# Performance work log

Hardware: AMD Instinct MI355X
Metric: run time of the kernel (lower is better)

## Reference

```python
import jax, jax.numpy as jnp
import numpy as np

N = 100000   # nodes
E = 1600000  # edges
G = 512      # graphs
ATOM = 64
HID = 64
CLS = 10


def layer_norm(x, g, b, eps=1e-5):
    mu = jnp.mean(x, axis=-1, keepdims=True)
    var = jnp.mean((x - mu) ** 2, axis=-1, keepdims=True)
    return (x - mu) * jax.lax.rsqrt(var + eps) * g + b


def gcn_conv(x, src, dst, W, b, fill, num_nodes):
    # PyG GCNConv with add_self_loops: A_hat = A + fill*I, sym-normalized.
    h = x @ W                                            # [N, F_out]
    ones = jnp.ones(src.shape[0], dtype=h.dtype)
    deg = jax.ops.segment_sum(ones, dst, num_segments=num_nodes) + fill
    dinv = jax.lax.rsqrt(deg)                            # deg^{-1/2}
    norm = dinv[src] * dinv[dst]                         # [E]
    msg = h[src] * norm[:, None]                         # gather + scale
    out = jax.ops.segment_sum(msg, dst, num_segments=num_nodes)
    out = out + (fill * dinv * dinv)[:, None] * h        # self-loop term
    return out + b


def setup_inputs() -> dict:
    key = jax.random.key(0)
    ks = jax.random.split(key, 8)
    x = jax.random.normal(ks[0], (N, ATOM), dtype=jnp.float32)
    edge_index = jax.random.randint(ks[1], (2, E), 0, N, dtype=jnp.int64)
    batch = jnp.sort(jax.random.randint(ks[2], (N,), 0, G, dtype=jnp.int64))
    s = lambda k, sh, fan: jax.random.normal(k, sh, jnp.float32) / np.sqrt(fan)
    return {
        "x": x, "edge_index": edge_index, "batch": batch,
        "W1": s(ks[3], (ATOM, HID), ATOM), "b1": jnp.zeros((HID,), jnp.float32),
        "ln_g": jnp.ones((HID,), jnp.float32), "ln_b": jnp.zeros((HID,), jnp.float32),
        "W2": s(ks[4], (HID, HID), HID), "b2": jnp.zeros((HID,), jnp.float32),
        "W3": s(ks[5], (HID, 768), HID), "b3": jnp.zeros((768,), jnp.float32),
        "ln2_g": jnp.ones((768,), jnp.float32), "ln2_b": jnp.zeros((768,), jnp.float32),
        "W4": s(ks[6], (768, CLS), 768), "b4": jnp.zeros((CLS,), jnp.float32),
    }


def reference(x, edge_index, batch, W1, b1, ln_g, ln_b, W2, b2,
              W3, b3, ln2_g, ln2_b, W4, b4):
    src, dst = edge_index[0], edge_index[1]
    leaky = lambda v: jax.nn.leaky_relu(v, 0.2)
    # GCN1 (improved=True -> self-loop weight 2.0) + LN + LeakyReLU
    h = gcn_conv(x, src, dst, W1, b1, 2.0, N)
    h = leaky(layer_norm(h, ln_g, ln_b))
    # GCN2 (self-loop weight 1.0) + LeakyReLU
    h = gcn_conv(h, src, dst, W2, b2, 1.0, N)
    h = leaky(h)
    # global max pool over graphs
    pooled = jax.ops.segment_max(h, batch, num_segments=G)  # [G, HID]
    # seq2 head (Dropout is identity at inference)
    z = pooled @ W3 + b3
    z = leaky(layer_norm(z, ln2_g, ln2_b))
    z = z @ W4 + b4
    return jax.nn.softmax(z, axis=-1)
```

## Files before the change

### kernel.cpp

```cpp
#include <hip/hip_runtime.h>
#include <hip/hip_bf16.h>

#define NODES 100000
#define EDGES 1600000
#define NGRAPH 512
#define NBINS 98
#define CHUNK 4096
#define VSS 72

using bf16 = __hip_bfloat16;
typedef long long ll;
using frag8 = __attribute__((ext_vector_type(8))) short;
using f32x4 = __attribute__((ext_vector_type(4))) float;

__device__ __forceinline__ float lrelu(float v) { return v > 0.0f ? v : 0.2f * v; }

__device__ __forceinline__ unsigned mapf(float f) {
    unsigned u = __float_as_uint(f);
    return (u & 0x80000000u) ? ~u : (u | 0x80000000u);
}
__device__ __forceinline__ float unmapf(unsigned u) {
    return __uint_as_float((u & 0x80000000u) ? (u ^ 0x80000000u) : ~u);
}

__device__ __forceinline__ int idx_at(const void* raw, int i, int f) {
    return f ? (int)((const ll*)raw)[i] : ((const int*)raw)[i];
}

__device__ __forceinline__ unsigned short tobf(float f) {
    bf16 h = __float2bfloat16(f);
    return *reinterpret_cast<unsigned short*>(&h);
}

__global__ void sentinel_kernel(float* out, float v) {
    int i = blockIdx.x * blockDim.x + threadIdx.x;
    if (i < NGRAPH * 10) out[i] = v;
}

__global__ void detect_init(const int* __restrict__ w, int* __restrict__ flag,
                            unsigned* __restrict__ pooled, int* __restrict__ binTotal,
                            int* __restrict__ binCursor) {
    int i = blockIdx.x * blockDim.x + threadIdx.x;
    if (i < NGRAPH * 64) pooled[i] = mapf(-1e4f);
    if (i < NBINS) { binTotal[i] = 0; binCursor[i] = 0; }
    if (blockIdx.x == 0) {
        __shared__ int red[4];
        int t = threadIdx.x;
        int v = 0;
        for (int k = t; k < 4096; k += 256) v |= w[2 * k + 1];
        for (int o = 32; o; o >>= 1) v |= __shfl_xor(v, o);
        if ((t & 63) == 0) red[t >> 6] = v;
        __syncthreads();
        if (t == 0) flag[0] = ((red[0] | red[1] | red[2] | red[3]) == 0) ? 1 : 0;
    }
}

__global__ void binCount(const void* __restrict__ ei, const int* __restrict__ flag,
                         int* __restrict__ binTotal) {
    __shared__ int hist[NBINS];
    int t = threadIdx.x;
    if (t < NBINS) hist[t] = 0;
    __syncthreads();
    int e0 = blockIdx.x * CHUNK;
    int f = flag[0];
#pragma unroll
    for (int k = 0; k < CHUNK / 256; ++k) {
        int i = e0 + k * 256 + t;
        if (i < EDGES) {
            int s = idx_at(ei, i, f), d = idx_at(ei, EDGES + i, f);
            if ((unsigned)s < NODES && (unsigned)d < NODES) atomicAdd(&hist[d >> 10], 1);
        }
    }
    __syncthreads();
    if (t < NBINS && hist[t] > 0) atomicAdd(&binTotal[t], hist[t]);
}

__global__ void scan98(const int* __restrict__ binTotal, int* __restrict__ binStart,
                       int* __restrict__ row_ptr) {
    __shared__ int sc[128];
    int t = threadIdx.x;
    int v = (t < NBINS) ? binTotal[t] : 0;
    sc[t] = v;
    __syncthreads();
    for (int o = 1; o < 128; o <<= 1) {
        int u = (t >= o) ? sc[t - o] : 0;
        __syncthreads();
        sc[t] += u;
        __syncthreads();
    }
    if (t < NBINS) binStart[t] = sc[t] - v;
    if (t == NBINS - 1) {
        binStart[NBINS] = sc[t];
        row_ptr[NODES] = sc[t];
    }
}

__global__ void binPlace(const void* __restrict__ ei, const int* __restrict__ flag,
                         const int* __restrict__ binStart, int* __restrict__ binCursor,
                         unsigned* __restrict__ staging) {
    __shared__ unsigned recs[CHUNK];
    __shared__ unsigned char binsA[CHUNK];
    __shared__ int hist[NBINS], lstart[NBINS + 1], baseg[NBINS], lcur[NBINS];
    int t = threadIdx.x;
    if (t < NBINS) { hist[t] = 0; lcur[t] = 0; }
    __syncthreads();
    int e0 = blockIdx.x * CHUNK;
    int f = flag[0];
#pragma unroll
    for (int k = 0; k < CHUNK / 256; ++k) {
        int i = e0 + k * 256 + t;
        if (i < EDGES) {
            int s = idx_at(ei, i, f), d = idx_at(ei, EDGES + i, f);
            if ((unsigned)s < NODES && (unsigned)d < NODES) atomicAdd(&hist[d >> 10], 1);
        }
    }
    __syncthreads();
    if (t == 0) {
        int acc = 0;
        for (int b = 0; b < NBINS; ++b) {
            lstart[b] = acc;
            acc += hist[b];
        }
        lstart[NBINS] = acc;
    }
    __syncthreads();
    if (t < NBINS && hist[t] > 0) baseg[t] = atomicAdd(&binCursor[t], hist[t]);
    __syncthreads();
#pragma unroll
    for (int k = 0; k < CHUNK / 256; ++k) {
        int i = e0 + k * 256 + t;
        if (i < EDGES) {
            int s = idx_at(ei, i, f), d = idx_at(ei, EDGES + i, f);
            if ((unsigned)s < NODES && (unsigned)d < NODES) {
                int b = d >> 10;
                int p = lstart[b] + atomicAdd(&lcur[b], 1);
                recs[p] = ((unsigned)s << 10) | (unsigned)(d & 1023);
                binsA[p] = (unsigned char)b;
            }
        }
    }
    __syncthreads();
    int nv = lstart[NBINS];
    for (int p = t; p < nv; p += 256) {
        int b = binsA[p];
        staging[binStart[b] + baseg[b] + (p - lstart[b])] = recs[p];
    }
}

__global__ void csr_finalize(const unsigned* __restrict__ staging,
                             const int* __restrict__ binStart, int* __restrict__ row_ptr,
                             float* __restrict__ dinv1, float* __restrict__ dinv2,
                             int* __restrict__ csr_src) {
    __shared__ int lhist[1024];
    __shared__ int sc[256];
    int b = blockIdx.x, t = threadIdx.x;
    int r0 = b << 10;
    int s0 = binStart[b], s1 = binStart[b + 1];
    for (int j = t; j < 1024; j += 256) lhist[j] = 0;
    __syncthreads();
    for (int p = s0 + t; p < s1; p += 256) atomicAdd(&lhist[staging[p] & 1023], 1);
    __syncthreads();
    int base = t * 4;
    int v0 = lhist[base], v1 = lhist[base + 1], v2 = lhist[base + 2], v3 = lhist[base + 3];
    int tsum = v0 + v1 + v2 + v3;
    sc[t] = tsum;
    __syncthreads();
    for (int o = 1; o < 256; o <<= 1) {
        int u = (t >= o) ? sc[t - o] : 0;
        __syncthreads();
        sc[t] += u;
        __syncthreads();
    }
    int excl = sc[t] - tsum;
    int vv0 = v0, vv1 = v1, vv2 = v2, vv3 = v3;
    int ex[4];
    ex[0] = excl;
    ex[1] = excl + vv0;
    ex[2] = ex[1] + vv1;
    ex[3] = ex[2] + vv2;
    int vvs[4] = {vv0, vv1, vv2, vv3};
#pragma unroll
    for (int k = 0; k < 4; ++k) {
        int j = base + k;
        int row = r0 + j;
        if (row < NODES) {
            row_ptr[row] = s0 + ex[k];
            float dg = (float)vvs[k];
            dinv1[row] = 1.0f / sqrtf(dg + 2.0f);
            dinv2[row] = 1.0f / sqrtf(dg + 1.0f);
        }
    }
    __syncthreads();
#pragma unroll
    for (int k = 0; k < 4; ++k) lhist[base + k] = ex[k];
    __syncthreads();
    for (int p = s0 + t; p < s1; p += 256) {
        unsigned rec = staging[p];
        int dl = rec & 1023;
        int slot = atomicAdd(&lhist[dl], 1);
        csr_src[s0 + slot] = (int)(rec >> 10);
    }
}

__global__ void prescale_x(const float* __restrict__ x, const float* __restrict__ dinv1,
                           bf16* __restrict__ xs) {
    int i = blockIdx.x * blockDim.x + threadIdx.x;
    if (i < NODES * 64) xs[i] = __float2bfloat16(x[i] * dinv1[i >> 6]);
}

__device__ __forceinline__ void gather_quad(const uint2* __restrict__ feat4,
                                            const int* __restrict__ csr, int beg, int end,
                                            int lane, float& ox, float& oy, float& oz,
                                            float& ow) {
    int q = lane >> 4, c = lane & 15;
    float ax = 0, ay = 0, az = 0, aw = 0;
    float bx = 0, by = 0, bz = 0, bw = 0;
    for (int cb = beg; cb < end; cb += 64) {
        int cnt = min(64, end - cb);
        int idx = (cb + lane < end) ? csr[cb + lane] : 0;
        for (int j = 0; j < cnt; j += 8) {
            int e0 = j + q, e1 = j + 4 + q;
            int s0 = __shfl(idx, e0);
            uint2 u0 = feat4[(size_t)s0 * 16 + c];
            if (e0 < cnt) {
                ax += __uint_as_float(u0.x << 16);
                ay += __uint_as_float(u0.x & 0xffff0000u);
                az += __uint_as_float(u0.y << 16);
                aw += __uint_as_float(u0.y & 0xffff0000u);
            }
            if (j + 4 < cnt) {
                int s1 = __shfl(idx, e1);
                uint2 u1 = feat4[(size_t)s1 * 16 + c];
                if (e1 < cnt) {
                    bx += __uint_as_float(u1.x << 16);
                    by += __uint_as_float(u1.x & 0xffff0000u);
                    bz += __uint_as_float(u1.y << 16);
                    bw += __uint_as_float(u1.y & 0xffff0000u);
                }
            }
        }
    }
    ax += bx; ay += by; az += bz; aw += bw;
    ax += __shfl_xor(ax, 16); ay += __shfl_xor(ay, 16);
    az += __shfl_xor(az, 16); aw += __shfl_xor(aw, 16);
    ax += __shfl_xor(ax, 32); ay += __shfl_xor(ay, 32);
    az += __shfl_xor(az, 32); aw += __shfl_xor(aw, 32);
    ox = ax; oy = ay; oz = az; ow = aw;
}

__device__ __forceinline__ void gcn_core(const uint2* __restrict__ feat4,
                                         const int* __restrict__ csr,
                                         const int* __restrict__ rp,
                                         const float* __restrict__ dinv, float selfw,
                                         const float* __restrict__ W, short* Vs, short* Wt,
                                         int rowBase, int lane, int wave, f32x4 (&acc)[4]) {
    int t = wave * 64 + lane;
    for (int i = t; i < 4096; i += 256) {
        int k = i >> 6, n = i & 63;
        Wt[n * VSS + k] = (short)tobf(W[i]);
    }
    __syncthreads();
    int myBase = rowBase + wave * 16;
    int rpv = (lane < 17) ? rp[min(myBase + lane, NODES)] : 0;
    int c = lane & 15;
    for (int i = 0; i < 16; ++i) {
        int beg = __shfl(rpv, i), end = __shfl(rpv, i + 1);
        float vx, vy, vz, vw;
        gather_quad(feat4, csr, beg, end, lane, vx, vy, vz, vw);
        int row = myBase + i;
        float dv = 0.0f;
        uint2 us = make_uint2(0u, 0u);
        if (row < NODES) {
            dv = dinv[row];
            us = feat4[(size_t)row * 16 + c];
        }
        vx = dv * (vx + selfw * __uint_as_float(us.x << 16));
        vy = dv * (vy + selfw * __uint_as_float(us.x & 0xffff0000u));
        vz = dv * (vz + selfw * __uint_as_float(us.y << 16));
        vw = dv * (vw + selfw * __uint_as_float(us.y & 0xffff0000u));
        if (lane < 16) {
            uint2 p;
            p.x = (unsigned)tobf(vx) | ((unsigned)tobf(vy) << 16);
            p.y = (unsigned)tobf(vz) | ((unsigned)tobf(vw) << 16);
            *(uint2*)(Vs + (size_t)(wave * 16 + i) * VSS + c * 4) = p;
        }
    }
    frag8 afr[2];
    int m = lane & 15, q = lane >> 4;
#pragma unroll
    for (int ks = 0; ks < 2; ++ks)
        afr[ks] = *(frag8*)(Vs + (size_t)(wave * 16 + m) * VSS + q * 8 + ks * 32);
#pragma unroll
    for (int nt = 0; nt < 4; ++nt) {
        f32x4 a = {0.f, 0.f, 0.f, 0.f};
#pragma unroll
        for (int ks = 0; ks < 2; ++ks) {
            frag8 bfr = *(frag8*)(Wt + (size_t)(nt * 16 + m) * VSS + q * 8 + ks * 32);
            a = __builtin_amdgcn_mfma_f32_16x16x32_bf16(afr[ks], bfr, a, 0, 0, 0);
        }
        acc[nt] = a;
    }
}

__global__ void __launch_bounds__(256, 2)
gcn1_fused(const uint2* __restrict__ xs4, const int* __restrict__ csr,
           const int* __restrict__ rp, const float* __restrict__ dinv1,
           const float* __restrict__ dinv2, const float* __restrict__ W1,
           const float* __restrict__ b1, const float* __restrict__ lng,
           const float* __restrict__ lnb, bf16* __restrict__ h1s) {
    __shared__ short sm[2 * 64 * VSS];
    short* Vs = sm;
    short* Wt = sm + 64 * VSS;
    int lane = threadIdx.x & 63, wave = threadIdx.x >> 6;
    int rowBase = blockIdx.x * 64;
    f32x4 acc[4];
    gcn_core(xs4, csr, rp, dinv1, 2.0f, W1, Vs, Wt, rowBase, lane, wave, acc);
    int c = lane & 15, q = lane >> 4;
    float bc[4], lg[4], lb[4];
#pragma unroll
    for (int nt = 0; nt < 4; ++nt) {
        bc[nt] = b1[nt * 16 + c];
        lg[nt] = lng[nt * 16 + c];
        lb[nt] = lnb[nt * 16 + c];
    }
#pragma unroll
    for (int r = 0; r < 4; ++r) {
        int grow = rowBase + wave * 16 + q * 4 + r;
        float v0 = acc[0][r] + bc[0], v1 = acc[1][r] + bc[1];
        float v2 = acc[2][r] + bc[2], v3 = acc[3][r] + bc[3];
        float s = v0 + v1 + v2 + v3;
        for (int o = 1; o < 16; o <<= 1) s += __shfl_xor(s, o);
        float mu = s * (1.0f / 64.0f);
        float d0 = v0 - mu, d1 = v1 - mu, d2 = v2 - mu, d3 = v3 - mu;
        float qq = d0 * d0 + d1 * d1 + d2 * d2 + d3 * d3;
        for (int o = 1; o < 16; o <<= 1) qq += __shfl_xor(qq, o);
        float rstd = 1.0f / sqrtf(qq * (1.0f / 64.0f) + 1e-5f);
        if (grow < NODES) {
            float d2v = dinv2[grow];
            bf16* dst = h1s + (size_t)grow * 64 + c;
            dst[0]  = __float2bfloat16(lrelu(d0 * rstd * lg[0] + lb[0]) * d2v);
            dst[16] = __float2bfloat16(lrelu(d1 * rstd * lg[1] + lb[1]) * d2v);
            dst[32] = __float2bfloat16(lrelu(d2 * rstd * lg[2] + lb[2]) * d2v);
            dst[48] = __float2bfloat16(lrelu(d3 * rstd * lg[3] + lb[3]) * d2v);
        }
    }
}

__global__ void __launch_bounds__(256, 2)
gcn2_fused(const uint2* __restrict__ h1s4, const int* __restrict__ csr,
           const int* __restrict__ rp, const float* __restrict__ dinv2,
           const float* __restrict__ W2, const float* __restrict__ b2,
           const void* __restrict__ batch, const int* __restrict__ flag,
           unsigned* __restrict__ pooled) {
    __shared__ short sm[2 * 64 * VSS];
    __shared__ int gsh[64];
    short* Vs = sm;
    short* Wt = sm + 64 * VSS;
    int t = threadIdx.x, lane = t & 63, wave = t >> 6;
    int rowBase = blockIdx.x * 64;
    if (t < 64) {
        int row = rowBase + t;
        gsh[t] = (row < NODES) ? idx_at(batch, row, flag[0]) : -1;
    }
    f32x4 acc[4];
    gcn_core(h1s4, csr, rp, dinv2, 1.0f, W2, Vs, Wt, rowBase, lane, wave, acc);
    int c = lane & 15, q = lane >> 4;
    float bc[4];
#pragma unroll
    for (int nt = 0; nt < 4; ++nt) bc[nt] = b2[nt * 16 + c];
    __syncthreads();
    float* P = (float*)sm;
#pragma unroll
    for (int r = 0; r < 4; ++r) {
        int mloc = wave * 16 + q * 4 + r;
#pragma unroll
        for (int nt = 0; nt < 4; ++nt)
            P[(size_t)mloc * 65 + nt * 16 + c] = lrelu(acc[nt][r] + bc[nt]);
    }
    __syncthreads();
    if (wave == 0) {
        float m = P[lane];
        int gc = gsh[0];
        for (int r = 1; r < 64; ++r) {
            int gr = gsh[r];
            float ar = P[(size_t)r * 65 + lane];
            if (gr == gc) {
                m = fmaxf(m, ar);
            } else {
                if ((unsigned)gc < NGRAPH) atomicMax(&pooled[gc * 64 + lane], mapf(m));
                gc = gr;
                m = ar;
            }
        }
        if ((unsigned)gc < NGRAPH) atomicMax(&pooled[gc * 64 + lane], mapf(m));
    }
}

__global__ void head_kernel(const unsigned* __restrict__ pooled, const float* __restrict__ W3,
                            const float* __restrict__ b3, const float* __restrict__ g2,
                            const float* __restrict__ be2, const float* __restrict__ W4,
                            const float* __restrict__ b4, float* __restrict__ out) {
    __shared__ float prow[64];
    __shared__ float z[768];
    __shared__ float rs[4], rss[4];
    __shared__ float mu_s, rstd_s;
    __shared__ float red[10];
    int t = threadIdx.x, gI = blockIdx.x;
    if (t < 64) prow[t] = unmapf(pooled[gI * 64 + t]);
    __syncthreads();
    for (int c = t; c < 768; c += 256) {
        float acc = b3[c];
#pragma unroll 16
        for (int k = 0; k < 64; ++k) acc += prow[k] * W3[k * 768 + c];
        z[c] = acc;
    }
    __syncthreads();
    float s = 0.0f, ss = 0.0f;
    for (int c = t; c < 768; c += 256) {
        float v = z[c];
        s += v;
        ss += v * v;
    }
    for (int o = 32; o; o >>= 1) {
        s += __shfl_xor(s, o);
        ss += __shfl_xor(ss, o);
    }
    if ((t & 63) == 0) { rs[t >> 6] = s; rss[t >> 6] = ss; }
    __syncthreads();
    if (t == 0) {
        float S = rs[0] + rs[1] + rs[2] + rs[3];
        float SS = rss[0] + rss[1] + rss[2] + rss[3];
        float mu = S * (1.0f / 768.0f);
        float var = SS * (1.0f / 768.0f) - mu * mu;
        mu_s = mu;
        rstd_s = 1.0f / sqrtf(fmaxf(var, 0.0f) + 1e-5f);
    }
    __syncthreads();
    for (int c = t; c < 768; c += 256) {
        float y = (z[c] - mu_s) * rstd_s * g2[c] + be2[c];
        z[c] = lrelu(y);
    }
    if (t < 10) red[t] = 0.0f;
    __syncthreads();
    float p[10];
#pragma unroll
    for (int c = 0; c < 10; ++c) p[c] = 0.0f;
    for (int k = t; k < 768; k += 256) {
        float zv = z[k];
#pragma unroll
        for (int c = 0; c < 10; ++c) p[c] += zv * W4[k * 10 + c];
    }
#pragma unroll
    for (int c = 0; c < 10; ++c) atomicAdd(&red[c], p[c]);
    __syncthreads();
    if (t == 0) {
        float l[10], m = -1e30f;
#pragma unroll
        for (int c = 0; c < 10; ++c) {
            l[c] = red[c] + b4[c];
            m = fmaxf(m, l[c]);
        }
        float sum = 0.0f;
#pragma unroll
        for (int c = 0; c < 10; ++c) {
            l[c] = expf(l[c] - m);
            sum += l[c];
        }
        float inv = 1.0f / sum;
#pragma unroll
        for (int c = 0; c < 10; ++c) out[gI * 10 + c] = l[c] * inv;
    }
}

extern "C" void kernel_launch(void* const* d_in, const int* in_sizes, int n_in,
                              void* d_out, int out_size, void* d_ws, size_t ws_size,
                              hipStream_t stream) {
    const size_t REQUIRED = (size_t)NODES * 64 * 2 * 2
                          + (size_t)EDGES * 4
                          + (size_t)(NODES + 1) * 4
                          + (size_t)NODES * 4 * 2
                          + (size_t)(NBINS * 3 + 1) * 4
                          + (size_t)NGRAPH * 64 * 4
                          + 16;
    if (ws_size < REQUIRED) {
        sentinel_kernel<<<20, 256, 0, stream>>>((float*)d_out, 64.0f);
        return;
    }

    const float* x = (const float*)d_in[0];
    const void* ei = d_in[1];
    const void* batch = d_in[2];
    const float* W1 = (const float*)d_in[3];
    const float* b1 = (const float*)d_in[4];
    const float* lng = (const float*)d_in[5];
    const float* lnb = (const float*)d_in[6];
    const float* W2 = (const float*)d_in[7];
    const float* b2 = (const float*)d_in[8];
    const float* W3 = (const float*)d_in[9];
    const float* b3 = (const float*)d_in[10];
    const float* g2 = (const float*)d_in[11];
    const float* be2 = (const float*)d_in[12];
    const float* W4 = (const float*)d_in[13];
    const float* b4 = (const float*)d_in[14];

    bf16* xs = (bf16*)d_ws;
    bf16* h1s = xs + (size_t)NODES * 64;
    unsigned* staging = (unsigned*)h1s;
    int* csr_src = (int*)(h1s + (size_t)NODES * 64);
    int* row_ptr = csr_src + EDGES;
    float* dinv1 = (float*)(row_ptr + NODES + 1);
    float* dinv2 = dinv1 + NODES;
    int* binTotal = (int*)(dinv2 + NODES);
    int* binStart = binTotal + NBINS;
    int* binCursor = binStart + NBINS + 1;
    unsigned* pooled = (unsigned*)(binCursor + NBINS);
    int* flag = (int*)(pooled + NGRAPH * 64);

    detect_init<<<(NGRAPH * 64 + 255) / 256, 256, 0, stream>>>((const int*)ei, flag, pooled,
                                                               binTotal, binCursor);

    int nchunks = (EDGES + CHUNK - 1) / CHUNK;
    binCount<<<nchunks, 256, 0, stream>>>(ei, flag, binTotal);
    scan98<<<1, 128, 0, stream>>>(binTotal, binStart, row_ptr);
    binPlace<<<nchunks, 256, 0, stream>>>(ei, flag, binStart, binCursor, staging);
    csr_finalize<<<NBINS, 256, 0, stream>>>(staging, binStart, row_ptr, dinv1, dinv2,
                                            csr_src);
    prescale_x<<<(NODES * 64 + 255) / 256, 256, 0, stream>>>(x, dinv1, xs);

    gcn1_fused<<<(NODES + 63) / 64, 256, 0, stream>>>((const uint2*)xs, csr_src, row_ptr,
                                                      dinv1, dinv2, W1, b1, lng, lnb, h1s);
    gcn2_fused<<<(NODES + 63) / 64, 256, 0, stream>>>((const uint2*)h1s, csr_src, row_ptr,
                                                      dinv2, W2, b2, batch, flag, pooled);

    head_kernel<<<NGRAPH, 256, 0, stream>>>(pooled, W3, b3, g2, be2, W4, b4, (float*)d_out);
}
```

Baseline: 330.0 us.

## Fuse CSR build stages, reuse chunk histograms, and gather two rows concurrently

The separate scan kernel is folded into binCount: the last block to finish, found with an atomic done-counter, computes the bin prefix sums. binCount also stores per-chunk histograms so binPlace no longer re-reads edges to count them. The x prescale kernel is merged into csr_finalize, and the init kernel becomes memsets plus a single-block flag kernel. The GCN gather now processes two destination rows at once to expose more memory-level parallelism. The cost is that the prescale work now runs on only 98 blocks, and more registers are used in the gather loop.

```diff
diff --git a/kernel.cpp b/kernel.cpp
--- a/kernel.cpp
+++ b/kernel.cpp
@@ -6,6 +6,7 @@
 #define NGRAPH 512
 #define NBINS 98
 #define CHUNK 4096
+#define NCHUNKS ((EDGES + CHUNK - 1) / CHUNK)
 #define VSS 72
 
 using bf16 = __hip_bfloat16;
@@ -37,27 +38,23 @@
     if (i < NGRAPH * 10) out[i] = v;
 }
 
-__global__ void detect_init(const int* __restrict__ w, int* __restrict__ flag,
-                            unsigned* __restrict__ pooled, int* __restrict__ binTotal,
-                            int* __restrict__ binCursor) {
-    int i = blockIdx.x * blockDim.x + threadIdx.x;
-    if (i < NGRAPH * 64) pooled[i] = mapf(-1e4f);
-    if (i < NBINS) { binTotal[i] = 0; binCursor[i] = 0; }
-    if (blockIdx.x == 0) {
-        __shared__ int red[4];
-        int t = threadIdx.x;
-        int v = 0;
-        for (int k = t; k < 4096; k += 256) v |= w[2 * k + 1];
-        for (int o = 32; o; o >>= 1) v |= __shfl_xor(v, o);
-        if ((t & 63) == 0) red[t >> 6] = v;
-        __syncthreads();
-        if (t == 0) flag[0] = ((red[0] | red[1] | red[2] | red[3]) == 0) ? 1 : 0;
-    }
+__global__ void flag_kernel(const int* __restrict__ w, int* __restrict__ flag) {
+    __shared__ int red[4];
+    int t = threadIdx.x;
+    int v = 0;
+    for (int k = t; k < 4096; k += 256) v |= w[2 * k + 1];
+    for (int o = 32; o; o >>= 1) v |= __shfl_xor(v, o);
+    if ((t & 63) == 0) red[t >> 6] = v;
+    __syncthreads();
+    if (t == 0) flag[0] = ((red[0] | red[1] | red[2] | red[3]) == 0) ? 1 : 0;
 }
 
 __global__ void binCount(const void* __restrict__ ei, const int* __restrict__ flag,
-                         int* __restrict__ binTotal) {
+                         int* __restrict__ binTotal, int* __restrict__ chunkHist,
+                         int* __restrict__ doneCtr, int* __restrict__ binStart,
+                         int* __restrict__ row_ptr) {
     __shared__ int hist[NBINS];
+    __shared__ int isLast;
     int t = threadIdx.x;
     if (t < NBINS) hist[t] = 0;
     __syncthreads();
@@ -72,47 +69,43 @@
         }
     }
     __syncthreads();
-    if (t < NBINS && hist[t] > 0) atomicAdd(&binTotal[t], hist[t]);
-}
-
-__global__ void scan98(const int* __restrict__ binTotal, int* __restrict__ binStart,
-                       int* __restrict__ row_ptr) {
-    __shared__ int sc[128];
-    int t = threadIdx.x;
-    int v = (t < NBINS) ? binTotal[t] : 0;
-    sc[t] = v;
-    __syncthreads();
-    for (int o = 1; o < 128; o <<= 1) {
-        int u = (t >= o) ? sc[t - o] : 0;
+    if (t < NBINS) {
+        chunkHist[blockIdx.x * NBINS + t] = hist[t];
+        if (hist[t] > 0) atomicAdd(&binTotal[t], hist[t]);
+    }
+    __threadfence();
+    if (t == 0) isLast = (atomicAdd(doneCtr, 1) == (int)gridDim.x - 1);
+    __syncthreads();
+    if (isLast) {
+        __threadfence();
+        __shared__ int sc[128];
+        int v = (t < NBINS) ? atomicAdd(&binTotal[t], 0) : 0;
+        if (t < 128) sc[t] = v;
         __syncthreads();
-        sc[t] += u;
-        __syncthreads();
-    }
-    if (t < NBINS) binStart[t] = sc[t] - v;
-    if (t == NBINS - 1) {
-        binStart[NBINS] = sc[t];
-        row_ptr[NODES] = sc[t];
+        for (int o = 1; o < 128; o <<= 1) {
+            int u = (t < 128 && t >= o) ? sc[t - o] : 0;
+            __syncthreads();
+            if (t < 128) sc[t] += u;
+            __syncthreads();
+        }
+        if (t < NBINS) binStart[t] = sc[t] - v;
+        if (t == NBINS - 1) {
+            binStart[NBINS] = sc[t];
+            row_ptr[NODES] = sc[t];
+        }
     }
 }
 
 __global__ void binPlace(const void* __restrict__ ei, const int* __restrict__ flag,
-                         const int* __restrict__ binStart, int* __restrict__ binCursor,
-                         unsigned* __restrict__ staging) {
+                         const int* __restrict__ chunkHist, const int* __restrict__ binStart,
+                         int* __restrict__ binCursor, unsigned* __restrict__ staging) {
     __shared__ unsigned recs[CHUNK];
     __shared__ unsigned char binsA[CHUNK];
     __shared__ int hist[NBINS], lstart[NBINS + 1], baseg[NBINS], lcur[NBINS];
     int t = threadIdx.x;
-    if (t < NBINS) { hist[t] = 0; lcur[t] = 0; }
-    __syncthreads();
-    int e0 = blockIdx.x * CHUNK;
-    int f = flag[0];
-#pragma unroll
-    for (int k = 0; k < CHUNK / 256; ++k) {
-        int i = e0 + k * 256 + t;
-        if (i < EDGES) {
-            int s = idx_at(ei, i, f), d = idx_at(ei, EDGES + i, f);
-            if ((unsigned)s < NODES && (unsigned)d < NODES) atomicAdd(&hist[d >> 10], 1);
-        }
+    if (t < NBINS) {
+        hist[t] = chunkHist[blockIdx.x * NBINS + t];
+        lcur[t] = 0;
     }
     __syncthreads();
     if (t == 0) {
@@ -126,6 +119,8 @@
     __syncthreads();
     if (t < NBINS && hist[t] > 0) baseg[t] = atomicAdd(&binCursor[t], hist[t]);
     __syncthreads();
+    int e0 = blockIdx.x * CHUNK;
+    int f = flag[0];
 #pragma unroll
     for (int k = 0; k < CHUNK / 256; ++k) {
         int i = e0 + k * 256 + t;
@@ -150,9 +145,11 @@
 __global__ void csr_finalize(const unsigned* __restrict__ staging,
                              const int* __restrict__ binStart, int* __restrict__ row_ptr,
                              float* __restrict__ dinv1, float* __restrict__ dinv2,
-                             int* __restrict__ csr_src) {
+                             int* __restrict__ csr_src, const float* __restrict__ x,
+                             bf16* __restrict__ xs) {
     __shared__ int lhist[1024];
     __shared__ int sc[256];
+    __shared__ float sdinv[1024];
     int b = blockIdx.x, t = threadIdx.x;
     int r0 = b << 10;
     int s0 = binStart[b], s1 = binStart[b + 1];
@@ -172,21 +169,22 @@
         __syncthreads();
     }
     int excl = sc[t] - tsum;
-    int vv0 = v0, vv1 = v1, vv2 = v2, vv3 = v3;
     int ex[4];
     ex[0] = excl;
-    ex[1] = excl + vv0;
-    ex[2] = ex[1] + vv1;
-    ex[3] = ex[2] + vv2;
-    int vvs[4] = {vv0, vv1, vv2, vv3};
+    ex[1] = excl + v0;
+    ex[2] = ex[1] + v1;
+    ex[3] = ex[2] + v2;
+    int vvs[4] = {v0, v1, v2, v3};
 #pragma unroll
     for (int k = 0; k < 4; ++k) {
         int j = base + k;
         int row = r0 + j;
+        float dg = (float)vvs[k];
+        float d1 = 1.0f / sqrtf(dg + 2.0f);
+        sdinv[j] = d1;
         if (row < NODES) {
             row_ptr[row] = s0 + ex[k];
-            float dg = (float)vvs[k];
-            dinv1[row] = 1.0f / sqrtf(dg + 2.0f);
+            dinv1[row] = d1;
             dinv2[row] = 1.0f / sqrtf(dg + 1.0f);
         }
     }
@@ -196,56 +194,97 @@
     __syncthreads();
     for (int p = s0 + t; p < s1; p += 256) {
         unsigned rec = staging[p];
-        int dl = rec & 1023;
-        int slot = atomicAdd(&lhist[dl], 1);
+        int slot = atomicAdd(&lhist[rec & 1023], 1);
         csr_src[s0 + slot] = (int)(rec >> 10);
     }
-}
-
-__global__ void prescale_x(const float* __restrict__ x, const float* __restrict__ dinv1,
-                           bf16* __restrict__ xs) {
-    int i = blockIdx.x * blockDim.x + threadIdx.x;
-    if (i < NODES * 64) xs[i] = __float2bfloat16(x[i] * dinv1[i >> 6]);
-}
-
-__device__ __forceinline__ void gather_quad(const uint2* __restrict__ feat4,
-                                            const int* __restrict__ csr, int beg, int end,
-                                            int lane, float& ox, float& oy, float& oz,
-                                            float& ow) {
+    for (int v = t; v < 1024 * 16; v += 256) {
+        int rl = v >> 4;
+        int row = r0 + rl;
+        if (row < NODES) {
+            float4 xv = ((const float4*)x)[(size_t)row * 16 + (v & 15)];
+            float d1 = sdinv[rl];
+            uint2 p;
+            p.x = (unsigned)tobf(xv.x * d1) | ((unsigned)tobf(xv.y * d1) << 16);
+            p.y = (unsigned)tobf(xv.z * d1) | ((unsigned)tobf(xv.w * d1) << 16);
+            ((uint2*)xs)[(size_t)row * 16 + (v & 15)] = p;
+        }
+    }
+}
+
+__device__ __forceinline__ void gather_quad2(
+    const uint2* __restrict__ feat4, const int* __restrict__ csr, int begA, int endA,
+    int begB, int endB, int lane, float& oxA, float& oyA, float& ozA, float& owA,
+    float& oxB, float& oyB, float& ozB, float& owB) {
     int q = lane >> 4, c = lane & 15;
-    float ax = 0, ay = 0, az = 0, aw = 0;
-    float bx = 0, by = 0, bz = 0, bw = 0;
-    for (int cb = beg; cb < end; cb += 64) {
-        int cnt = min(64, end - cb);
-        int idx = (cb + lane < end) ? csr[cb + lane] : 0;
-        for (int j = 0; j < cnt; j += 8) {
+    float a1x = 0, a1y = 0, a1z = 0, a1w = 0, a2x = 0, a2y = 0, a2z = 0, a2w = 0;
+    float b1x = 0, b1y = 0, b1z = 0, b1w = 0, b2x = 0, b2y = 0, b2z = 0, b2w = 0;
+    int cbA = begA, cbB = begB;
+    while (cbA < endA || cbB < endB) {
+        int cntA = endA - cbA;
+        cntA = cntA > 64 ? 64 : (cntA < 0 ? 0 : cntA);
+        int cntB = endB - cbB;
+        cntB = cntB > 64 ? 64 : (cntB < 0 ? 0 : cntB);
+        int idxA = (lane < cntA) ? csr[cbA + lane] : 0;
+        int idxB = (lane < cntB) ? csr[cbB + lane] : 0;
+        int jm = cntA > cntB ? cntA : cntB;
+        for (int j = 0; j < jm; j += 8) {
             int e0 = j + q, e1 = j + 4 + q;
-            int s0 = __shfl(idx, e0);
-            uint2 u0 = feat4[(size_t)s0 * 16 + c];
-            if (e0 < cnt) {
-                ax += __uint_as_float(u0.x << 16);
-                ay += __uint_as_float(u0.x & 0xffff0000u);
-                az += __uint_as_float(u0.y << 16);
-                aw += __uint_as_float(u0.y & 0xffff0000u);
-            }
-            if (j + 4 < cnt) {
-                int s1 = __shfl(idx, e1);
-                uint2 u1 = feat4[(size_t)s1 * 16 + c];
-                if (e1 < cnt) {
-                    bx += __uint_as_float(u1.x << 16);
-                    by += __uint_as_float(u1.x & 0xffff0000u);
-                    bz += __uint_as_float(u1.y << 16);
-                    bw += __uint_as_float(u1.y & 0xffff0000u);
+            if (j < cntA) {
+                int sA0 = __shfl(idxA, e0);
+                uint2 uA0 = feat4[(size_t)sA0 * 16 + c];
+                if (e0 < cntA) {
+                    a1x += __uint_as_float(uA0.x << 16);
+                    a1y += __uint_as_float(uA0.x & 0xffff0000u);
+                    a1z += __uint_as_float(uA0.y << 16);
+                    a1w += __uint_as_float(uA0.y & 0xffff0000u);
+                }
+                if (j + 4 < cntA) {
+                    int sA1 = __shfl(idxA, e1);
+                    uint2 uA1 = feat4[(size_t)sA1 * 16 + c];
+                    if (e1 < cntA) {
+                        a2x += __uint_as_float(uA1.x << 16);
+                        a2y += __uint_as_float(uA1.x & 0xffff0000u);
+                        a2z += __uint_as_float(uA1.y << 16);
+                        a2w += __uint_as_float(uA1.y & 0xffff0000u);
+                    }
                 }
             }
-        }
-    }
-    ax += bx; ay += by; az += bz; aw += bw;
-    ax += __shfl_xor(ax, 16); ay += __shfl_xor(ay, 16);
-    az += __shfl_xor(az, 16); aw += __shfl_xor(aw, 16);
-    ax += __shfl_xor(ax, 32); ay += __shfl_xor(ay, 32);
-    az += __shfl_xor(az, 32); aw += __shfl_xor(aw, 32);
-    ox = ax; oy = ay; oz = az; ow = aw;
+            if (j < cntB) {
+                int sB0 = __shfl(idxB, e0);
+                uint2 uB0 = feat4[(size_t)sB0 * 16 + c];
+                if (e0 < cntB) {
+                    b1x += __uint_as_float(uB0.x << 16);
+                    b1y += __uint_as_float(uB0.x & 0xffff0000u);
+                    b1z += __uint_as_float(uB0.y << 16);
+                    b1w += __uint_as_float(uB0.y & 0xffff0000u);
+                }
+                if (j + 4 < cntB) {
+                    int sB1 = __shfl(idxB, e1);
+                    uint2 uB1 = feat4[(size_t)sB1 * 16 + c];
+                    if (e1 < cntB) {
+                        b2x += __uint_as_float(uB1.x << 16);
+                        b2y += __uint_as_float(uB1.x & 0xffff0000u);
+                        b2z += __uint_as_float(uB1.y << 16);
+                        b2w += __uint_as_float(uB1.y & 0xffff0000u);
+                    }
+                }
+            }
+        }
+        cbA += 64;
+        cbB += 64;
+    }
+    a1x += a2x; a1y += a2y; a1z += a2z; a1w += a2w;
+    b1x += b2x; b1y += b2y; b1z += b2z; b1w += b2w;
+    a1x += __shfl_xor(a1x, 16); a1y += __shfl_xor(a1y, 16);
+    a1z += __shfl_xor(a1z, 16); a1w += __shfl_xor(a1w, 16);
+    b1x += __shfl_xor(b1x, 16); b1y += __shfl_xor(b1y, 16);
+    b1z += __shfl_xor(b1z, 16); b1w += __shfl_xor(b1w, 16);
+    a1x += __shfl_xor(a1x, 32); a1y += __shfl_xor(a1y, 32);
+    a1z += __shfl_xor(a1z, 32); a1w += __shfl_xor(a1w, 32);
+    b1x += __shfl_xor(b1x, 32); b1y += __shfl_xor(b1y, 32);
+    b1z += __shfl_xor(b1z, 32); b1w += __shfl_xor(b1w, 32);
+    oxA = a1x; oyA = a1y; ozA = a1z; owA = a1w;
+    oxB = b1x; oyB = b1y; ozB = b1z; owB = b1w;
 }
 
 __device__ __forceinline__ void gcn_core(const uint2* __restrict__ feat4,
@@ -263,26 +302,40 @@
     int myBase = rowBase + wave * 16;
     int rpv = (lane < 17) ? rp[min(myBase + lane, NODES)] : 0;
     int c = lane & 15;
-    for (int i = 0; i < 16; ++i) {
-        int beg = __shfl(rpv, i), end = __shfl(rpv, i + 1);
-        float vx, vy, vz, vw;
-        gather_quad(feat4, csr, beg, end, lane, vx, vy, vz, vw);
-        int row = myBase + i;
-        float dv = 0.0f;
-        uint2 us = make_uint2(0u, 0u);
-        if (row < NODES) {
-            dv = dinv[row];
-            us = feat4[(size_t)row * 16 + c];
-        }
-        vx = dv * (vx + selfw * __uint_as_float(us.x << 16));
-        vy = dv * (vy + selfw * __uint_as_float(us.x & 0xffff0000u));
-        vz = dv * (vz + selfw * __uint_as_float(us.y << 16));
-        vw = dv * (vw + selfw * __uint_as_float(us.y & 0xffff0000u));
+    for (int ii = 0; ii < 8; ++ii) {
+        int iA = ii, iB = ii + 8;
+        int begA = __shfl(rpv, iA), endA = __shfl(rpv, iA + 1);
+        int begB = __shfl(rpv, iB), endB = __shfl(rpv, iB + 1);
+        float vxA, vyA, vzA, vwA, vxB, vyB, vzB, vwB;
+        gather_quad2(feat4, csr, begA, endA, begB, endB, lane, vxA, vyA, vzA, vwA, vxB,
+                     vyB, vzB, vwB);
+        int rowA = myBase + iA, rowB = myBase + iB;
+        float dvA = 0.0f, dvB = 0.0f;
+        uint2 usA = make_uint2(0u, 0u), usB = make_uint2(0u, 0u);
+        if (rowA < NODES) {
+            dvA = dinv[rowA];
+            usA = feat4[(size_t)rowA * 16 + c];
+        }
+        if (rowB < NODES) {
+            dvB = dinv[rowB];
+            usB = feat4[(size_t)rowB * 16 + c];
+        }
+        vxA = dvA * (vxA + selfw * __uint_as_float(usA.x << 16));
+        vyA = dvA * (vyA + selfw * __uint_as_float(usA.x & 0xffff0000u));
+        vzA = dvA * (vzA + selfw * __uint_as_float(usA.y << 16));
+        vwA = dvA * (vwA + selfw * __uint_as_float(usA.y & 0xffff0000u));
+        vxB = dvB * (vxB + selfw * __uint_as_float(usB.x << 16));
+        vyB = dvB * (vyB + selfw * __uint_as_float(usB.x & 0xffff0000u));
+        vzB = dvB * (vzB + selfw * __uint_as_float(usB.y << 16));
+        vwB = dvB * (vwB + selfw * __uint_as_float(usB.y & 0xffff0000u));
         if (lane < 16) {
-            uint2 p;
-            p.x = (unsigned)tobf(vx) | ((unsigned)tobf(vy) << 16);
-            p.y = (unsigned)tobf(vz) | ((unsigned)tobf(vw) << 16);
-            *(uint2*)(Vs + (size_t)(wave * 16 + i) * VSS + c * 4) = p;
+            uint2 pA, pB;
+            pA.x = (unsigned)tobf(vxA) | ((unsigned)tobf(vyA) << 16);
+            pA.y = (unsigned)tobf(vzA) | ((unsigned)tobf(vwA) << 16);
+            pB.x = (unsigned)tobf(vxB) | ((unsigned)tobf(vyB) << 16);
+            pB.y = (unsigned)tobf(vzB) | ((unsigned)tobf(vwB) << 16);
+            *(uint2*)(Vs + (size_t)(wave * 16 + iA) * VSS + c * 4) = pA;
+            *(uint2*)(Vs + (size_t)(wave * 16 + iB) * VSS + c * 4) = pB;
         }
     }
     frag8 afr[2];
@@ -479,7 +532,8 @@
                           + (size_t)EDGES * 4
                           + (size_t)(NODES + 1) * 4
                           + (size_t)NODES * 4 * 2
-                          + (size_t)(NBINS * 3 + 1) * 4
+                          + (size_t)(NBINS * 3 + 2) * 4
+                          + (size_t)NCHUNKS * NBINS * 4
                           + (size_t)NGRAPH * 64 * 4
                           + 16;
     if (ws_size < REQUIRED) {
@@ -511,21 +565,22 @@
     float* dinv1 = (float*)(row_ptr + NODES + 1);
     float* dinv2 = dinv1 + NODES;
     int* binTotal = (int*)(dinv2 + NODES);
-    int* binStart = binTotal + NBINS;
-    int* binCursor = binStart + NBINS + 1;
-    unsigned* pooled = (unsigned*)(binCursor + NBINS);
+    int* binCursor = binTotal + NBINS;
+    int* doneCtr = binCursor + NBINS;
+    int* binStart = doneCtr + 1;
+    int* chunkHist = binStart + NBINS + 1;
+    unsigned* pooled = (unsigned*)(chunkHist + NCHUNKS * NBINS);
     int* flag = (int*)(pooled + NGRAPH * 64);
 
-    detect_init<<<(NGRAPH * 64 + 255) / 256, 256, 0, stream>>>((const int*)ei, flag, pooled,
-                                                               binTotal, binCursor);
-
-    int nchunks = (EDGES + CHUNK - 1) / CHUNK;
-    binCount<<<nchunks, 256, 0, stream>>>(ei, flag, binTotal);
-    scan98<<<1, 128, 0, stream>>>(binTotal, binStart, row_ptr);
-    binPlace<<<nchunks, 256, 0, stream>>>(ei, flag, binStart, binCursor, staging);
+    hipMemsetAsync(binTotal, 0, (size_t)(NBINS * 2 + 1) * 4, stream);
+    hipMemsetAsync(pooled, 0, (size_t)NGRAPH * 64 * 4, stream);
+    flag_kernel<<<1, 256, 0, stream>>>((const int*)ei, flag);
+
+    binCount<<<NCHUNKS, 256, 0, stream>>>(ei, flag, binTotal, chunkHist, doneCtr, binStart,
+                                          row_ptr);
+    binPlace<<<NCHUNKS, 256, 0, stream>>>(ei, flag, chunkHist, binStart, binCursor, staging);
     csr_finalize<<<NBINS, 256, 0, stream>>>(staging, binStart, row_ptr, dinv1, dinv2,
-                                            csr_src);
-    prescale_x<<<(NODES * 64 + 255) / 256, 256, 0, stream>>>(x, dinv1, xs);
+                                            csr_src, x, xs);
 
     gcn1_fused<<<(NODES + 63) / 64, 256, 0, stream>>>((const uint2*)xs, csr_src, row_ptr,
                                                       dinv1, dinv2, W1, b1, lng, lnb, h1s);
```

After: 359.5 us. 8.9% more time.
